# Kernel tuning notes

Hardware: AMD Instinct MI355X
Metric: run time of the kernel (lower is better)

## Reference

```python
import jax, jax.numpy as jnp
import numpy as np

B, N, NPOINT, NSAMPLE, C = 8, 8192, 2048, 32, 64
RADIUS = 0.2
MLP = [C + 3, 64, 64, 128]  # use_xyz=True -> C+3 input channels


def setup_inputs() -> dict:
    key = jax.random.key(0)
    ks = jax.random.split(key, 8)
    xyz = jax.random.normal(ks[0], (B, N, 3), jnp.float32)
    features = jax.random.normal(ks[1], (B, C, N), jnp.float32)
    inp = {"xyz": xyz, "features": features}
    # shared-MLP (1x1 conv) weights, He-init
    for i in range(3):
        cin, cout = MLP[i], MLP[i + 1]
        scale = jnp.sqrt(jnp.float32(2.0) / cin)
        inp[f"W{i+1}"] = jax.random.normal(ks[2 + i], (cout, cin), jnp.float32) * scale
        inp[f"b{i+1}"] = jnp.zeros((cout,), jnp.float32)
    return inp


def furthest_point_sample(xyz, npoint):
    # xyz: (B, N, 3) -> idx: (B, npoint). Greedy FPS, seeded at point 0 (as CUDA impl).
    b, n, _ = xyz.shape

    def step(carry, _):
        dist, far = carry  # dist: (B, N) running min dist-to-set; far: (B,)
        centroid = jnp.take_along_axis(xyz, far[:, None, None], axis=1)  # (B,1,3)
        d = jnp.sum((xyz - centroid) ** 2, axis=-1)  # (B, N)
        dist = jnp.minimum(dist, d)
        nxt = jnp.argmax(dist, axis=-1).astype(jnp.int32)
        return (dist, nxt), far

    init = (jnp.full((b, n), jnp.inf, xyz.dtype), jnp.zeros((b,), jnp.int32))
    _, idx = jax.lax.scan(step, init, None, length=npoint)  # (npoint, B)
    return idx.T  # (B, npoint)


def ball_query(xyz, new_xyz, radius, nsample):
    # xyz: (B,N,3), new_xyz: (B,S,3) -> idx: (B,S,nsample)
    n = xyz.shape[1]
    d2 = jnp.sum((new_xyz[:, :, None, :] - xyz[:, None, :, :]) ** 2, axis=-1)  # (B,S,N)
    inball = d2 < jnp.float32(radius) ** 2
    keys = jnp.where(inball, jnp.arange(n, dtype=jnp.int32), jnp.int32(n))
    neg_small, _ = jax.lax.top_k(-keys, nsample)  # nsample smallest indices in ball
    idx = -neg_small  # (B,S,nsample), padded with n where fewer than nsample
    first = idx[..., :1]
    idx = jnp.where(idx == n, first, idx)  # repeat first valid neighbor (CUDA semantics)
    idx = jnp.where(idx == n, 0, idx)  # empty ball -> index 0
    return idx


def reference(xyz, features, W1, b1, W2, b2, W3, b3):
    # --- sample: FPS + gather centers (non-differentiable index selection) ---
    fps_idx = furthest_point_sample(jax.lax.stop_gradient(xyz), NPOINT)  # (B,S)
    new_xyz = jnp.take_along_axis(xyz, fps_idx[:, :, None], axis=1)  # (B,S,3)

    # --- group: ball query + gather neighbors, relative coords, concat feats ---
    idx = ball_query(jax.lax.stop_gradient(xyz), jax.lax.stop_gradient(new_xyz),
                     RADIUS, NSAMPLE)  # (B,S,K)
    batch_ix = jnp.arange(B)[:, None, None]
    grouped_xyz = xyz[batch_ix, idx] - new_xyz[:, :, None, :]  # (B,S,K,3)
    feats_n = jnp.swapaxes(features, 1, 2)  # (B,N,C)
    grouped_feats = feats_n[batch_ix, idx]  # (B,S,K,C)
    x = jnp.concatenate([grouped_xyz, grouped_feats], axis=-1)  # (B,S,K,C+3)

    # --- shared MLP (1x1 convs + ReLU) ---
    x = jax.nn.relu(jnp.einsum('bskc,oc->bsko', x, W1) + b1)
    x = jax.nn.relu(jnp.einsum('bskc,oc->bsko', x, W2) + b2)
    x = jax.nn.relu(jnp.einsum('bskc,oc->bsko', x, W3) + b3)

    # --- max-pool over neighborhood K ---
    new_features = jnp.max(x, axis=2)  # (B,S,out)
    new_features = jnp.swapaxes(new_features, 1, 2)  # (B,out,S)
    return new_xyz, new_features
```

## Files before the change

kernel.cpp:

```cpp
#include <hip/hip_runtime.h>

#define BB 8
#define NN 8192
#define NPOINT 2048
#define NSAMPLE 32
#define CC 64

typedef float v2f __attribute__((ext_vector_type(2)));

__global__ __launch_bounds__(256) void k_transpose(const float* __restrict__ f,
                                                   float* __restrict__ ft) {
  __shared__ float tile[64][65];
  int b = blockIdx.y;
  int p0 = blockIdx.x * 64;
  int tx = threadIdx.x, ty = threadIdx.y;
  const float* fb = f + (size_t)b * CC * NN;
#pragma unroll
  for (int i = 0; i < 16; ++i) {
    int c = i * 4 + ty;
    tile[c][tx] = fb[(size_t)c * NN + p0 + tx];
  }
  __syncthreads();
  float* fo = ft + ((size_t)b * NN + p0) * CC;
#pragma unroll
  for (int i = 0; i < 16; ++i) {
    int pl = i * 4 + ty;
    fo[(size_t)pl * CC + tx] = tile[tx][pl];
  }
}

__global__ void k_permW1(const float* __restrict__ W1, float* __restrict__ W1p) {
  int i = blockIdx.x * 256 + threadIdx.x;
  if (i < 64 * 68) {
    int o = i / 68, k = i % 68;
    float v;
    if (k < 64) v = W1[o * 67 + 3 + k];
    else if (k < 67) v = W1[o * 67 + (k - 64)];
    else v = 0.0f;
    W1p[i] = v;
  }
}

#define DPPMAX(var, ctrl)                                                       \
  {                                                                             \
    unsigned long long _b = (unsigned long long)__double_as_longlong(var);      \
    int _lo = __builtin_amdgcn_update_dpp(0, (int)(unsigned)_b, ctrl, 0xf, 0xf, \
                                          false);                               \
    int _hi = __builtin_amdgcn_update_dpp(0, (int)(unsigned)(_b >> 32), ctrl,   \
                                          0xf, 0xf, false);                     \
    double _s = __longlong_as_double(                                           \
        (long long)(((unsigned long long)(unsigned)_hi << 32) | (unsigned)_lo));\
    var = fmax(var, _s);                                                        \
  }

__global__ __launch_bounds__(512, 2) void k_fps(const float* __restrict__ xyz,
                                                float* __restrict__ newxyz) {
  __shared__ __align__(16) float4 sxyz[NN];
  __shared__ float swin[3 * NPOINT];
  __shared__ __align__(16) double wkey[2][8];
  int b = blockIdx.x;
  const float* X = xyz + (size_t)b * NN * 3;
  int t = threadIdx.x;
  int lane = t & 63;
  v2f px[8], py[8], pz[8], dd[8];
#pragma unroll
  for (int j = 0; j < 8; ++j) {
    int p0 = t + (2 * j) * 512, p1 = p0 + 512;
    float x0 = X[p0 * 3 + 0], y0 = X[p0 * 3 + 1], z0 = X[p0 * 3 + 2];
    float x1 = X[p1 * 3 + 0], y1 = X[p1 * 3 + 1], z1 = X[p1 * 3 + 2];
    px[j].x = x0; px[j].y = x1;
    py[j].x = y0; py[j].y = y1;
    pz[j].x = z0; pz[j].y = z1;
    sxyz[p0] = make_float4(x0, y0, z0, 0.0f);
    sxyz[p1] = make_float4(x1, y1, z1, 0.0f);
    dd[j].x = __builtin_inff(); dd[j].y = __builtin_inff();
  }
  __syncthreads();
  float cx, cy, cz;
  {
    float4 c0 = sxyz[0];
    cx = c0.x; cy = c0.y; cz = c0.z;
  }
  if (t == 0) { swin[0] = cx; swin[1] = cy; swin[2] = cz; }
  for (int it = 1; it < NPOINT; ++it) {
#pragma clang fp contract(off)
    v2f vcx, vcy, vcz;
    vcx.x = cx; vcx.y = cx;
    vcy.x = cy; vcy.y = cy;
    vcz.x = cz; vcz.y = cz;
    float m0 = -1.0f, m1 = -1.0f;
    int k0 = 0, k1 = 0;
#pragma unroll
    for (int j = 0; j < 8; ++j) {
      v2f dx = px[j] - vcx;
      v2f dy = py[j] - vcy;
      v2f dz = pz[j] - vcz;
      v2f xx = dx * dx;
      v2f yy = dy * dy;
      v2f zz = dz * dz;
      v2f s = xx + yy;
      v2f d = s + zz;
      v2f nd = __builtin_elementwise_min(dd[j], d);
      dd[j] = nd;
      if (nd.x > m0) { m0 = nd.x; k0 = j; }
      if (nd.y > m1) { m1 = nd.y; k1 = j; }
    }
    unsigned i0 = (unsigned)(t + (k0 << 10));
    unsigned i1 = (unsigned)(t + (k1 << 10) + 512);
    double best = __longlong_as_double(
        (long long)(((unsigned long long)__float_as_uint(m0) << 32) | ~i0));
    double c1 = __longlong_as_double(
        (long long)(((unsigned long long)__float_as_uint(m1) << 32) | ~i1));
    best = fmax(best, c1);
    DPPMAX(best, 0x111)
    DPPMAX(best, 0x112)
    DPPMAX(best, 0x114)
    DPPMAX(best, 0x118)
    DPPMAX(best, 0x142)
    DPPMAX(best, 0x143)
    int sel = it & 1;
    if (lane == 63) wkey[sel][t >> 6] = best;
    __syncthreads();
    double gk = wkey[sel][lane & 7];
    DPPMAX(gk, 0xB1)
    DPPMAX(gk, 0x4E)
    DPPMAX(gk, 0x124)
    unsigned wi = ~(unsigned)(unsigned long long)__double_as_longlong(gk);
    float4 cw = sxyz[wi];
    cx = cw.x; cy = cw.y; cz = cw.z;
    if (t == 0) {
      swin[3 * it + 0] = cx;
      swin[3 * it + 1] = cy;
      swin[3 * it + 2] = cz;
    }
  }
  __syncthreads();
  float* ob = newxyz + (size_t)b * 3 * NPOINT;
#pragma unroll
  for (int i = 0; i < 12; ++i) ob[t + i * 512] = swin[t + i * 512];
}

__global__ __launch_bounds__(256) void k_mlp(
    const float* __restrict__ featsT, const float* __restrict__ xyz,
    const float* __restrict__ newxyz,
    const float* __restrict__ W1p, const float* __restrict__ b1,
    const float* __restrict__ W2, const float* __restrict__ b2,
    const float* __restrict__ W3, const float* __restrict__ b3,
    float* __restrict__ outf) {
  __shared__ __align__(16) float xb[4][32][68];
  __shared__ int lidx[4][32];
  int w = threadIdx.x >> 6, lane = threadIdx.x & 63;
  int g = blockIdx.x * 4 + w;
  int b = g >> 11, s2 = g & 2047;
  const float* X = xyz + (size_t)b * NN * 3;
  const float* cp = newxyz + (((size_t)b << 11) + s2) * 3;
  float ccx = cp[0], ccy = cp[1], ccz = cp[2];

  {
    const float r2 = 0.2f * 0.2f;
    int found = 0;
    for (int ch = 0; ch < NN / 64; ++ch) {
      int p = ch * 64 + lane;
      float x = X[p * 3 + 0], y = X[p * 3 + 1], z = X[p * 3 + 2];
      float dx = __fsub_rn(ccx, x);
      float dy = __fsub_rn(ccy, y);
      float dz = __fsub_rn(ccz, z);
      float d2 = __fadd_rn(__fadd_rn(__fmul_rn(dx, dx), __fmul_rn(dy, dy)),
                           __fmul_rn(dz, dz));
      bool in = d2 < r2;
      unsigned long long m = __ballot(in);
      int rank = __popcll(m & ((1ull << lane) - 1ull));
      int slot = found + rank;
      if (in && slot < NSAMPLE) lidx[w][slot] = p;
      found += __popcll(m);
      if (found >= NSAMPLE) break;
    }
    int nf = found < NSAMPLE ? found : NSAMPLE;
    int sl = lane & 31, half = lane >> 5;
    int p = (nf == 0) ? 0 : lidx[w][sl < nf ? sl : 0];
    const float4* src = (const float4*)(featsT + (((size_t)b << 13) + p) * 64);
    float4* dst = (float4*)&xb[w][sl][0];
    if (half == 0) {
#pragma unroll
      for (int kt = 0; kt < 8; ++kt) dst[kt] = src[kt];
    } else {
#pragma unroll
      for (int kt = 8; kt < 16; ++kt) dst[kt] = src[kt];
      const float* pp = X + p * 3;
      float dx = __fsub_rn(pp[0], ccx);
      float dy = __fsub_rn(pp[1], ccy);
      float dz = __fsub_rn(pp[2], ccz);
      dst[16] = make_float4(dx, dy, dz, 0.0f);
    }
  }
  int si = lane & 3, oi = lane >> 2;
  float* xrow0 = &xb[w][0][0];
  float acc[4][8];

#pragma unroll
  for (int r = 0; r < 4; ++r) {
    float bv = b1[oi * 4 + r];
#pragma unroll
    for (int q = 0; q < 8; ++q) acc[r][q] = bv;
  }
  for (int kt = 0; kt < 17; ++kt) {
    float4 wv[4];
#pragma unroll
    for (int r = 0; r < 4; ++r)
      wv[r] = *(const float4*)(W1p + (oi * 4 + r) * 68 + kt * 4);
#pragma unroll
    for (int q = 0; q < 8; ++q) {
      float4 xv = *(const float4*)(xrow0 + (si + 4 * q) * 68 + kt * 4);
#pragma unroll
      for (int r = 0; r < 4; ++r) {
        acc[r][q] = fmaf(wv[r].x, xv.x, acc[r][q]);
        acc[r][q] = fmaf(wv[r].y, xv.y, acc[r][q]);
        acc[r][q] = fmaf(wv[r].z, xv.z, acc[r][q]);
        acc[r][q] = fmaf(wv[r].w, xv.w, acc[r][q]);
      }
    }
  }
#pragma unroll
  for (int q = 0; q < 8; ++q) {
    int s = si + 4 * q;
    float4 v = make_float4(fmaxf(acc[0][q], 0.f), fmaxf(acc[1][q], 0.f),
                           fmaxf(acc[2][q], 0.f), fmaxf(acc[3][q], 0.f));
    *(float4*)(xrow0 + s * 68 + oi * 4) = v;
  }

#pragma unroll
  for (int r = 0; r < 4; ++r) {
    float bv = b2[oi * 4 + r];
#pragma unroll
    for (int q = 0; q < 8; ++q) acc[r][q] = bv;
  }
  for (int kt = 0; kt < 16; ++kt) {
    float4 wv[4];
#pragma unroll
    for (int r = 0; r < 4; ++r)
      wv[r] = *(const float4*)(W2 + (oi * 4 + r) * 64 + kt * 4);
#pragma unroll
    for (int q = 0; q < 8; ++q) {
      float4 xv = *(const float4*)(xrow0 + (si + 4 * q) * 68 + kt * 4);
#pragma unroll
      for (int r = 0; r < 4; ++r) {
        acc[r][q] = fmaf(wv[r].x, xv.x, acc[r][q]);
        acc[r][q] = fmaf(wv[r].y, xv.y, acc[r][q]);
        acc[r][q] = fmaf(wv[r].z, xv.z, acc[r][q]);
        acc[r][q] = fmaf(wv[r].w, xv.w, acc[r][q]);
      }
    }
  }
#pragma unroll
  for (int q = 0; q < 8; ++q) {
    int s = si + 4 * q;
    float4 v = make_float4(fmaxf(acc[0][q], 0.f), fmaxf(acc[1][q], 0.f),
                           fmaxf(acc[2][q], 0.f), fmaxf(acc[3][q], 0.f));
    *(float4*)(xrow0 + s * 68 + oi * 4) = v;
  }

  float accB[4][8];
#pragma unroll
  for (int r = 0; r < 4; ++r) {
    float bvA = b3[oi * 4 + r];
    float bvB = b3[64 + oi * 4 + r];
#pragma unroll
    for (int q = 0; q < 8; ++q) { acc[r][q] = bvA; accB[r][q] = bvB; }
  }
  for (int kt = 0; kt < 16; ++kt) {
    float4 wa[4], wb[4];
#pragma unroll
    for (int r = 0; r < 4; ++r) {
      wa[r] = *(const float4*)(W3 + (oi * 4 + r) * 64 + kt * 4);
      wb[r] = *(const float4*)(W3 + (64 + oi * 4 + r) * 64 + kt * 4);
    }
#pragma unroll
    for (int q = 0; q < 8; ++q) {
      float4 xv = *(const float4*)(xrow0 + (si + 4 * q) * 68 + kt * 4);
#pragma unroll
      for (int r = 0; r < 4; ++r) {
        acc[r][q] = fmaf(wa[r].x, xv.x, acc[r][q]);
        acc[r][q] = fmaf(wa[r].y, xv.y, acc[r][q]);
        acc[r][q] = fmaf(wa[r].z, xv.z, acc[r][q]);
        acc[r][q] = fmaf(wa[r].w, xv.w, acc[r][q]);
        accB[r][q] = fmaf(wb[r].x, xv.x, accB[r][q]);
        accB[r][q] = fmaf(wb[r].y, xv.y, accB[r][q]);
        accB[r][q] = fmaf(wb[r].z, xv.z, accB[r][q]);
        accB[r][q] = fmaf(wb[r].w, xv.w, accB[r][q]);
      }
    }
  }
#pragma unroll
  for (int r = 0; r < 4; ++r) {
    float mA = acc[r][0], mB = accB[r][0];
#pragma unroll
    for (int q = 1; q < 8; ++q) {
      mA = fmaxf(mA, acc[r][q]);
      mB = fmaxf(mB, accB[r][q]);
    }
    mA = fmaxf(mA, __shfl_xor(mA, 1));
    mA = fmaxf(mA, __shfl_xor(mA, 2));
    mB = fmaxf(mB, __shfl_xor(mB, 1));
    mB = fmaxf(mB, __shfl_xor(mB, 2));
    mA = fmaxf(mA, 0.0f);
    mB = fmaxf(mB, 0.0f);
    if (si == 0) {
      int o = oi * 4 + r;
      outf[(((size_t)b * 128 + o) << 11) + s2] = mA;
      outf[(((size_t)b * 128 + o + 64) << 11) + s2] = mB;
    }
  }
}

extern "C" void kernel_launch(void* const* d_in, const int* in_sizes, int n_in,
                              void* d_out, int out_size, void* d_ws, size_t ws_size,
                              hipStream_t stream) {
  const float* xyz = (const float*)d_in[0];
  const float* feats = (const float*)d_in[1];
  const float* W1 = (const float*)d_in[2];
  const float* b1 = (const float*)d_in[3];
  const float* W2 = (const float*)d_in[4];
  const float* b2 = (const float*)d_in[5];
  const float* W3 = (const float*)d_in[6];
  const float* b3 = (const float*)d_in[7];
  float* out_newxyz = (float*)d_out;
  float* out_feats = (float*)d_out + (size_t)BB * NPOINT * 3;

  char* ws = (char*)d_ws;
  float* featsT = (float*)ws;
  float* W1p = (float*)(ws + 16777216);

  dim3 tb(64, 4);
  k_transpose<<<dim3(NN / 64, BB), tb, 0, stream>>>(feats, featsT);
  k_permW1<<<17, 256, 0, stream>>>(W1, W1p);
  k_fps<<<BB, 512, 0, stream>>>(xyz, out_newxyz);
  k_mlp<<<(BB * NPOINT) / 4, 256, 0, stream>>>(featsT, xyz, out_newxyz,
                                               W1p, b1, W2, b2, W3, b3, out_feats);
}
```

Measured before the change: 2.085 ms.

## Halve FPS block to 256 threads with 32 points each and inline packed asm

The furthest-point-sampling kernel now runs 4 waves per block instead of 8. Each thread holds 32 points in registers instead of 16, and the cross-wave reduction drops one DPP step. The distance computation is written as inline v_pk_add/v_pk_mul assembly using negated centroids, which keeps the no-contraction rounding. The aim is to cut per-iteration barrier and reduction latency in the serial 2048-step loop, in exchange for doubling the per-thread ALU work and register pressure.

```diff
diff --git a/kernel.cpp b/kernel.cpp
--- a/kernel.cpp
+++ b/kernel.cpp
@@ -53,19 +53,19 @@
     var = fmax(var, _s);                                                        \
   }
 
-__global__ __launch_bounds__(512, 2) void k_fps(const float* __restrict__ xyz,
+__global__ __launch_bounds__(256, 1) void k_fps(const float* __restrict__ xyz,
                                                 float* __restrict__ newxyz) {
   __shared__ __align__(16) float4 sxyz[NN];
   __shared__ float swin[3 * NPOINT];
-  __shared__ __align__(16) double wkey[2][8];
+  __shared__ __align__(16) double wkey[2][4];
   int b = blockIdx.x;
   const float* X = xyz + (size_t)b * NN * 3;
   int t = threadIdx.x;
   int lane = t & 63;
-  v2f px[8], py[8], pz[8], dd[8];
-#pragma unroll
-  for (int j = 0; j < 8; ++j) {
-    int p0 = t + (2 * j) * 512, p1 = p0 + 512;
+  v2f px[16], py[16], pz[16], dd[16];
+#pragma unroll
+  for (int j = 0; j < 16; ++j) {
+    int p0 = t + (2 * j) * 256, p1 = p0 + 256;
     float x0 = X[p0 * 3 + 0], y0 = X[p0 * 3 + 1], z0 = X[p0 * 3 + 2];
     float x1 = X[p1 * 3 + 0], y1 = X[p1 * 3 + 1], z1 = X[p1 * 3 + 2];
     px[j].x = x0; px[j].y = x1;
@@ -84,29 +84,36 @@
   if (t == 0) { swin[0] = cx; swin[1] = cy; swin[2] = cz; }
   for (int it = 1; it < NPOINT; ++it) {
 #pragma clang fp contract(off)
-    v2f vcx, vcy, vcz;
-    vcx.x = cx; vcx.y = cx;
-    vcy.x = cy; vcy.y = cy;
-    vcz.x = cz; vcz.y = cz;
+    float ncx = -cx, ncy = -cy, ncz = -cz;
+    v2f ncx2, ncy2, ncz2;
+    ncx2.x = ncx; ncx2.y = ncx;
+    ncy2.x = ncy; ncy2.y = ncy;
+    ncz2.x = ncz; ncz2.y = ncz;
     float m0 = -1.0f, m1 = -1.0f;
     int k0 = 0, k1 = 0;
 #pragma unroll
-    for (int j = 0; j < 8; ++j) {
-      v2f dx = px[j] - vcx;
-      v2f dy = py[j] - vcy;
-      v2f dz = pz[j] - vcz;
-      v2f xx = dx * dx;
-      v2f yy = dy * dy;
-      v2f zz = dz * dz;
-      v2f s = xx + yy;
-      v2f d = s + zz;
-      v2f nd = __builtin_elementwise_min(dd[j], d);
+    for (int j = 0; j < 16; ++j) {
+      v2f d, yy, zz;
+      asm("v_pk_add_f32 %0, %3, %6\n\t"
+          "v_pk_add_f32 %1, %4, %7\n\t"
+          "v_pk_add_f32 %2, %5, %8\n\t"
+          "v_pk_mul_f32 %0, %0, %0\n\t"
+          "v_pk_mul_f32 %1, %1, %1\n\t"
+          "v_pk_mul_f32 %2, %2, %2\n\t"
+          "v_pk_add_f32 %0, %0, %1\n\t"
+          "v_pk_add_f32 %0, %0, %2"
+          : "=&v"(d), "=&v"(yy), "=&v"(zz)
+          : "v"(px[j]), "v"(py[j]), "v"(pz[j]), "v"(ncx2), "v"(ncy2),
+            "v"(ncz2));
+      v2f nd;
+      nd.x = fminf(dd[j].x, d.x);
+      nd.y = fminf(dd[j].y, d.y);
       dd[j] = nd;
       if (nd.x > m0) { m0 = nd.x; k0 = j; }
       if (nd.y > m1) { m1 = nd.y; k1 = j; }
     }
-    unsigned i0 = (unsigned)(t + (k0 << 10));
-    unsigned i1 = (unsigned)(t + (k1 << 10) + 512);
+    unsigned i0 = (unsigned)(t + (k0 << 9));
+    unsigned i1 = (unsigned)(t + (k1 << 9) + 256);
     double best = __longlong_as_double(
         (long long)(((unsigned long long)__float_as_uint(m0) << 32) | ~i0));
     double c1 = __longlong_as_double(
@@ -121,10 +128,9 @@
     int sel = it & 1;
     if (lane == 63) wkey[sel][t >> 6] = best;
     __syncthreads();
-    double gk = wkey[sel][lane & 7];
+    double gk = wkey[sel][lane & 3];
     DPPMAX(gk, 0xB1)
     DPPMAX(gk, 0x4E)
-    DPPMAX(gk, 0x124)
     unsigned wi = ~(unsigned)(unsigned long long)__double_as_longlong(gk);
     float4 cw = sxyz[wi];
     cx = cw.x; cy = cw.y; cz = cw.z;
@@ -137,7 +143,7 @@
   __syncthreads();
   float* ob = newxyz + (size_t)b * 3 * NPOINT;
 #pragma unroll
-  for (int i = 0; i < 12; ++i) ob[t + i * 512] = swin[t + i * 512];
+  for (int i = 0; i < 24; ++i) ob[t + i * 256] = swin[t + i * 256];
 }
 
 __global__ __launch_bounds__(256) void k_mlp(
@@ -333,7 +339,7 @@
   dim3 tb(64, 4);
   k_transpose<<<dim3(NN / 64, BB), tb, 0, stream>>>(feats, featsT);
   k_permW1<<<17, 256, 0, stream>>>(W1, W1p);
-  k_fps<<<BB, 512, 0, stream>>>(xyz, out_newxyz);
+  k_fps<<<BB, 256, 0, stream>>>(xyz, out_newxyz);
   k_mlp<<<(BB * NPOINT) / 4, 256, 0, stream>>>(featsT, xyz, out_newxyz,
                                                W1p, b1, W2, b2, W3, b3, out_feats);
 }
```

Result: slower. 2.140 ms (+2.6%).
